# Kernel tuning notes

Measured on AMD Instinct MI355X. Metric: run time of the kernel, lower is better.

Reference implementation:

```python
import jax, jax.numpy as jnp
import numpy as np

N_NODES = 256
N_BAGS = 4
BAG_SIZE = 64


def _conv1d(x, w, b):
    # x: [B, C, T], w: [O, I, K], 'same' padding (pad=1, k=3), stride 1
    y = jax.lax.conv_general_dilated(x, w, window_strides=(1,), padding=[(1, 1)],
                                     dimension_numbers=('NCH', 'OIH', 'NCH'))
    return y + b[None, :, None]


def _select_indices(attention, degree):
    # Deterministic analogue of subgraphSelection: top-4 nodes by degree; for each,
    # prob row hrl = (row + row) * 100 (original numpy graph[:][b] is also row b);
    # pick 64 globally-distinct indices (collision avoidance) by probability, sorted.
    _, b4 = jax.lax.top_k(degree, N_BAGS)
    taken = jnp.zeros(N_NODES, dtype=bool)
    rows = []
    for i in range(N_BAGS):  # fixed small loop
        probs = 200.0 * attention[b4[i]]
        masked = jnp.where(taken, -jnp.inf, probs)
        _, idx = jax.lax.top_k(masked, BAG_SIZE)
        idx = jnp.sort(idx)
        taken = taken.at[idx].set(True)
        rows.append(idx)
    return jnp.stack(rows)  # [4, 64] int32


def setup_inputs() -> dict:
    key = jax.random.key(0)
    ks = jax.random.split(key, 13)
    B, T = 32768, N_NODES
    return {
        'attention': jax.random.uniform(ks[0], (N_NODES, N_NODES), jnp.float32),
        'degree': jax.random.uniform(ks[1], (N_NODES,), jnp.float32),
        'x': jax.random.normal(ks[2], (B, T, 1), jnp.float32),
        'conv1_w': jax.random.normal(ks[3], (1, 1, 3), jnp.float32) * 0.01,
        'conv1_b': jnp.zeros((1,), jnp.float32),
        'W1': jax.random.normal(ks[4], (64, 64), jnp.float32) * 0.05,
        'b1': jnp.zeros((64,), jnp.float32),
        'W2': jax.random.normal(ks[5], (64, 64), jnp.float32) * 0.05,
        'b2': jnp.zeros((64,), jnp.float32),
        'Wa': jax.random.normal(ks[6], (64, 64), jnp.float32) * 0.05,
        'ba': jnp.zeros((64,), jnp.float32),
        'conv2_w': jax.random.normal(ks[7], (4, 4, 3), jnp.float32) * 0.01,
        'conv2_b': jnp.zeros((4,), jnp.float32),
    }


def reference(attention, degree, x, conv1_w, conv1_b, W1, b1, W2, b2, Wa, ba, conv2_w, conv2_b):
    idx = _select_indices(attention, degree)            # [4, 64]
    xp = jnp.transpose(x, (0, 2, 1))                    # [B, 1, T]
    # Conv1D_feature_extracter(1,1,3): tanh(dropout(tanh(conv))) -> eval-mode tanh(tanh(conv))
    x_site = jnp.tanh(jnp.tanh(_conv1d(xp, conv1_w, conv1_b)))  # [B, 1, T]
    # mapping_converge: irregular gather x[b, 0, idx] -> [B, 4, 64]
    mx = xp[:, 0, :][:, idx]
    # IMILmask (torch Linear: y = x W^T + b)
    l1 = jax.nn.relu(mx @ W1.T + b1)
    l2 = jax.nn.relu(mx @ W2.T + b2)
    A_imi = jax.nn.sigmoid((l1 + l2) @ Wa.T + ba)
    masked_x = (A_imi + 1.0) * mx                       # [B, 4, 64]
    # Conv1D_feature_extracter(4,4,3)
    x_bag = jnp.tanh(jnp.tanh(_conv1d(masked_x, conv2_w, conv2_b)))  # [B, 4, 64]
    return (x_bag, x_site)
```

## Files before the change

### kernel.cpp

```cpp
#include <hip/hip_runtime.h>
#include <hip/hip_bf16.h>
#include <math.h>


#define NB 16

typedef __bf16 bf16x8 __attribute__((ext_vector_type(8)));
typedef float  f32x4  __attribute__((ext_vector_type(4)));

__device__ __forceinline__ float tanh_poly(float y) {
    float y2 = y * y;
    float p = fmaf(y2, -0.008863829f, 0.021869488f);
    p = fmaf(y2, p, -0.053968254f);
    p = fmaf(y2, p, 0.13333334f);
    p = fmaf(y2, p, -0.33333334f);
    p = fmaf(y2, p, 1.0f);
    return y * p;
}
__device__ __forceinline__ float dtanh2(float y) { return tanh_poly(tanh_poly(y)); }

__global__ __launch_bounds__(1024) void sel_kernel(
    const float* __restrict__ att, const float* __restrict__ deg,
    int* __restrict__ permg)
{
    __shared__ float pv[256];
    __shared__ int taken[256];
    __shared__ int part[256][5];
    __shared__ int b4s[4];
    __shared__ unsigned long long wmask[4];

    const int tid  = threadIdx.x;
    const int j    = tid & 255;
    const int q    = tid >> 8;
    const int lane = tid & 63;
    const int wv   = tid >> 6;

    if (tid < 256) { taken[tid] = 0; pv[tid] = deg[tid]; }
    __syncthreads();

    for (int rnd = -1; rnd < 4; ++rnd) {
        if (rnd >= 0) {
            if (tid < 256) {
                float p = 200.0f * att[b4s[rnd] * 256 + tid];
                pv[tid] = taken[tid] ? -__builtin_huge_valf() : p;
            }
            __syncthreads();
        }
        {
            float pj = pv[j];
            int cnt = 0;
            const int base = q * 64;
            #pragma unroll 4
            for (int k0 = 0; k0 < 64; ++k0) {
                int k = base + k0;
                float pk = pv[k];
                cnt += (pk > pj || (pk == pj && k < j)) ? 1 : 0;
            }
            part[j][q] = cnt;
        }
        __syncthreads();
        int sel = 0;
        if (tid < 256) {
            int rank = part[tid][0] + part[tid][1] + part[tid][2] + part[tid][3];
            if (rnd < 0) {
                if (rank < 4) b4s[rank] = tid;
            } else {
                sel = (rank < 64) ? 1 : 0;
            }
        }
        if (rnd >= 0) {
            unsigned long long mask = __ballot(sel);
            if (lane == 0 && wv < 4) wmask[wv] = mask;
            __syncthreads();
            if (sel) {
                int pos = __popcll(mask & ((1ull << lane) - 1ull));
                #pragma unroll
                for (int w = 0; w < 4; ++w) if (w < wv) pos += __popcll(wmask[w]);
                permg[rnd * 64 + pos] = tid;
                taken[tid] = 1;
            }
        }
        __syncthreads();
    }
}

__global__ __launch_bounds__(256, 2) void main_kernel(
    const float* __restrict__ x,
    const float* __restrict__ c1w, const float* __restrict__ c1b,
    const float* __restrict__ W1,  const float* __restrict__ b1,
    const float* __restrict__ W2,  const float* __restrict__ b2,
    const float* __restrict__ Wa,  const float* __restrict__ ba,
    const float* __restrict__ c2w, const float* __restrict__ c2b,
    const int* __restrict__ permg,
    float* __restrict__ out, int Btot)
{
    __shared__ float xls[NB][264];
    __shared__ bf16x8 w12f[8][2][64];
    __shared__ bf16x8 w3f[4][2][64];
    __shared__ int perm[256];
    __shared__ __align__(16) unsigned char scratch[4][4352];

    const int tid = threadIdx.x;
    const int batch0 = blockIdx.x * NB;

    #pragma unroll
    for (int i = 0; i < 4; ++i) {
        int flat = i * 1024 + tid * 4;
        int r = flat >> 8, c = flat & 255;
        const float4 v = *(const float4*)&x[(size_t)(batch0 + r) * 256 + c];
        *(float4*)&xls[r][c] = v;
    }
    #pragma unroll
    for (int ii = 0; ii < 4; ++ii) {
        int id = tid + 256 * ii;
        int ct = id >> 7, h = (id >> 6) & 1, l2 = id & 63;
        int n = ct * 16 + (l2 & 15);
        int k = h * 32 + (l2 >> 4) * 8;
        const float* src = (n < 64) ? (W1 + n * 64 + k) : (W2 + (n - 64) * 64 + k);
        float4 u = *(const float4*)src;
        float4 v = *(const float4*)(src + 4);
        bf16x8 f;
        f[0]=(__bf16)u.x; f[1]=(__bf16)u.y; f[2]=(__bf16)u.z; f[3]=(__bf16)u.w;
        f[4]=(__bf16)v.x; f[5]=(__bf16)v.y; f[6]=(__bf16)v.z; f[7]=(__bf16)v.w;
        w12f[ct][h][l2] = f;
    }
    #pragma unroll
    for (int ii = 0; ii < 2; ++ii) {
        int id = tid + 256 * ii;
        int ct = id >> 7, h = (id >> 6) & 1, l2 = id & 63;
        int n = ct * 16 + (l2 & 15);
        int k = h * 32 + (l2 >> 4) * 8;
        const float* src = Wa + n * 64 + k;
        float4 u = *(const float4*)src;
        float4 v = *(const float4*)(src + 4);
        bf16x8 f;
        f[0]=(__bf16)u.x; f[1]=(__bf16)u.y; f[2]=(__bf16)u.z; f[3]=(__bf16)u.w;
        f[4]=(__bf16)v.x; f[5]=(__bf16)v.y; f[6]=(__bf16)v.z; f[7]=(__bf16)v.w;
        w3f[ct][h][l2] = f;
    }
    perm[tid & 255] = permg[tid & 255];
    __syncthreads();

    {
        const float cw0 = c1w[0], cw1 = c1w[1], cw2 = c1w[2], cb = c1b[0];
        const size_t siteBase = (size_t)Btot * 256;
        #pragma unroll
        for (int i = 0; i < 4; ++i) {
            int flat = i * 1024 + tid * 4;
            int r = flat >> 8, c = flat & 255;
            const float* xr = &xls[r][0];
            float xm = (c > 0)       ? xr[c - 1] : 0.0f;
            float x0 = xr[c], x1 = xr[c + 1], x2 = xr[c + 2], x3 = xr[c + 3];
            float xp = (c + 4 < 256) ? xr[c + 4] : 0.0f;
            float4 o4;
            o4.x = dtanh2(fmaf(cw0, xm, fmaf(cw1, x0, fmaf(cw2, x1, cb))));
            o4.y = dtanh2(fmaf(cw0, x0, fmaf(cw1, x1, fmaf(cw2, x2, cb))));
            o4.z = dtanh2(fmaf(cw0, x1, fmaf(cw1, x2, fmaf(cw2, x3, cb))));
            o4.w = dtanh2(fmaf(cw0, x2, fmaf(cw1, x3, fmaf(cw2, xp, cb))));
            *(float4*)&out[siteBase + (size_t)(batch0 + r) * 256 + c] = o4;
        }
    }

    const int l = tid & 63, wvi = tid >> 6;
    const int hi = l >> 4, m = l & 15;

    float b1v[4], b2v[4], bav[4];
    #pragma unroll
    for (int ct = 0; ct < 4; ++ct) {
        b1v[ct] = b1[ct * 16 + m];
        b2v[ct] = b2[ct * 16 + m];
        bav[ct] = ba[ct * 16 + m];
    }

    const int bag = m & 3;
    const int bL  = wvi * 4 + (m >> 2);
    bf16x8 af0, af1;
    #pragma unroll
    for (int jj = 0; jj < 8; ++jj) {
        int k0 = hi * 8 + jj;
        af0[jj] = (__bf16)xls[bL][perm[bag * 64 + k0]];
        af1[jj] = (__bf16)xls[bL][perm[bag * 64 + 32 + k0]];
    }

    f32x4 acc12[8];
    #pragma unroll
    for (int ct = 0; ct < 8; ++ct) acc12[ct] = (f32x4){0.f, 0.f, 0.f, 0.f};
    #pragma unroll
    for (int ct = 0; ct < 8; ++ct) {
        acc12[ct] = __builtin_amdgcn_mfma_f32_16x16x32_bf16(af0, w12f[ct][0][l], acc12[ct], 0, 0, 0);
        acc12[ct] = __builtin_amdgcn_mfma_f32_16x16x32_bf16(af1, w12f[ct][1][l], acc12[ct], 0, 0, 0);
    }

    __bf16* lsb = (__bf16*)scratch[wvi];
    #pragma unroll
    for (int ct = 0; ct < 4; ++ct) {
        #pragma unroll
        for (int qq = 0; qq < 4; ++qq) {
            float a = acc12[ct][qq] + b1v[ct];      a = a > 0.f ? a : 0.f;
            float b = acc12[ct + 4][qq] + b2v[ct];  b = b > 0.f ? b : 0.f;
            lsb[(hi * 4 + qq) * 72 + ct * 16 + m] = (__bf16)(a + b);
        }
    }
    bf16x8 a30 = *(const bf16x8*)(lsb + m * 72 + hi * 8);
    bf16x8 a31 = *(const bf16x8*)(lsb + m * 72 + 32 + hi * 8);

    f32x4 acc3[4];
    #pragma unroll
    for (int ct = 0; ct < 4; ++ct) acc3[ct] = (f32x4){0.f, 0.f, 0.f, 0.f};
    #pragma unroll
    for (int ct = 0; ct < 4; ++ct) {
        acc3[ct] = __builtin_amdgcn_mfma_f32_16x16x32_bf16(a30, w3f[ct][0][l], acc3[ct], 0, 0, 0);
        acc3[ct] = __builtin_amdgcn_mfma_f32_16x16x32_bf16(a31, w3f[ct][1][l], acc3[ct], 0, 0, 0);
    }

    __syncthreads();

    float* msk = (float*)scratch[wvi];
    #pragma unroll
    for (int ct = 0; ct < 4; ++ct) {
        #pragma unroll
        for (int qq = 0; qq < 4; ++qq) {
            float v = acc3[ct][qq] + bav[ct];
            float s = __builtin_amdgcn_rcpf(1.0f + __expf(-v)) + 1.0f;
            int r  = hi * 4 + qq;
            int bq = r >> 2, ii = r & 3;
            int t  = ct * 16 + m;
            float mxv = xls[wvi * 4 + bq][perm[ii * 64 + t]];
            msk[(bq * 4 + ii) * 68 + t] = s * mxv;
        }
    }

    {
        const int bq2 = m >> 2, o = m & 3;
        const int tseg = hi * 16;
        float wv2[4][3];
        #pragma unroll
        for (int ii = 0; ii < 4; ++ii)
            #pragma unroll
            for (int kk = 0; kk < 3; ++kk)
                wv2[ii][kk] = c2w[o * 12 + ii * 3 + kk];
        const float cb2 = c2b[o];

        float mrow[4][16], mm1[4], mp1[4];
        #pragma unroll
        for (int ii = 0; ii < 4; ++ii) {
            const float* base = msk + (bq2 * 4 + ii) * 68;
            #pragma unroll
            for (int ch = 0; ch < 4; ++ch) {
                float4 vv = *(const float4*)(base + tseg + ch * 4);
                mrow[ii][ch * 4 + 0] = vv.x; mrow[ii][ch * 4 + 1] = vv.y;
                mrow[ii][ch * 4 + 2] = vv.z; mrow[ii][ch * 4 + 3] = vv.w;
            }
            mm1[ii] = (tseg > 0)       ? base[tseg - 1]  : 0.0f;
            mp1[ii] = (tseg + 16 < 64) ? base[tseg + 16] : 0.0f;
        }

        float res[16];
        #pragma unroll
        for (int t = 0; t < 16; ++t) {
            float a = cb2;
            #pragma unroll
            for (int ii = 0; ii < 4; ++ii) {
                float xm = (t == 0)  ? mm1[ii] : mrow[ii][t - 1];
                float xc = mrow[ii][t];
                float xp = (t == 15) ? mp1[ii] : mrow[ii][t + 1];
                a = fmaf(wv2[ii][0], xm, a);
                a = fmaf(wv2[ii][1], xc, a);
                a = fmaf(wv2[ii][2], xp, a);
            }
            res[t] = dtanh2(a);
        }
        float* op = out + (size_t)(batch0 + wvi * 4 + bq2) * 256 + o * 64 + tseg;
        #pragma unroll
        for (int ch = 0; ch < 4; ++ch) {
            float4 o4 = { res[ch*4+0], res[ch*4+1], res[ch*4+2], res[ch*4+3] };
            *(float4*)(op + ch * 4) = o4;
        }
    }
}

extern "C" void kernel_launch(void* const* d_in, const int* in_sizes, int n_in,
                              void* d_out, int out_size, void* d_ws, size_t ws_size,
                              hipStream_t stream)
{
    const float* att = (const float*)d_in[0];
    const float* deg = (const float*)d_in[1];
    const float* x   = (const float*)d_in[2];
    const float* c1w = (const float*)d_in[3];
    const float* c1b = (const float*)d_in[4];
    const float* W1  = (const float*)d_in[5];
    const float* b1  = (const float*)d_in[6];
    const float* W2  = (const float*)d_in[7];
    const float* b2  = (const float*)d_in[8];
    const float* Wa  = (const float*)d_in[9];
    const float* ba  = (const float*)d_in[10];
    const float* c2w = (const float*)d_in[11];
    const float* c2b = (const float*)d_in[12];
    float* out = (float*)d_out;
    int* perm  = (int*)d_ws;
    int Btot   = in_sizes[2] / 256;

    hipLaunchKernelGGL(sel_kernel, dim3(1), dim3(1024), 0, stream, att, deg, perm);
    hipLaunchKernelGGL(main_kernel, dim3(Btot / NB), dim3(256), 0, stream,
                       x, c1w, c1b, W1, b1, W2, b2, Wa, ba, c2w, c2b,
                       perm, out, Btot);
}
```

Baseline: 157.6 us.

## Precompute bf16 weight fragments once in prologue kernel, read from global in main

Moves the per-block fp32-to-bf16 conversion of W1/W2/Wa into a second block of the selection kernel, which writes pre-swizzled MFMA fragments to workspace. The main kernel reads the B fragments directly from global/L2 instead of staging them in LDS. This removes redundant conversion work and about 24KB of LDS per block, and the launch bound rises to 4 blocks per CU. The selection kernel's rank loop also now reads LDS as float4. The cost is that MFMA operands now come from global loads through cache, which may add latency. The workspace must also be large enough to hold the fragments.

```diff
diff --git a/kernel.cpp b/kernel.cpp
--- a/kernel.cpp
+++ b/kernel.cpp
@@ -19,17 +19,48 @@
 }
 __device__ __forceinline__ float dtanh2(float y) { return tanh_poly(tanh_poly(y)); }
 
+__device__ __forceinline__ bf16x8 cvt_frag(const float* src) {
+    float4 u = *(const float4*)src;
+    float4 v = *(const float4*)(src + 4);
+    bf16x8 f;
+    f[0]=(__bf16)u.x; f[1]=(__bf16)u.y; f[2]=(__bf16)u.z; f[3]=(__bf16)u.w;
+    f[4]=(__bf16)v.x; f[5]=(__bf16)v.y; f[6]=(__bf16)v.z; f[7]=(__bf16)v.w;
+    return f;
+}
+
 __global__ __launch_bounds__(1024) void sel_kernel(
     const float* __restrict__ att, const float* __restrict__ deg,
+    const float* __restrict__ W1, const float* __restrict__ W2,
+    const float* __restrict__ Wa,
     int* __restrict__ permg)
 {
-    __shared__ float pv[256];
+    const int tid = threadIdx.x;
+
+    if (blockIdx.x == 1) {
+        bf16x8* w12g = (bf16x8*)(permg + 256);
+        bf16x8* w3g  = w12g + 1024;
+        {
+            int ct = tid >> 7, h = (tid >> 6) & 1, l2 = tid & 63;
+            int n = ct * 16 + (l2 & 15);
+            int k = h * 32 + (l2 >> 4) * 8;
+            const float* src = (n < 64) ? (W1 + n * 64 + k) : (W2 + (n - 64) * 64 + k);
+            w12g[ct * 128 + h * 64 + l2] = cvt_frag(src);
+        }
+        if (tid < 512) {
+            int ct = tid >> 7, h = (tid >> 6) & 1, l2 = tid & 63;
+            int n = ct * 16 + (l2 & 15);
+            int k = h * 32 + (l2 >> 4) * 8;
+            w3g[ct * 128 + h * 64 + l2] = cvt_frag(Wa + n * 64 + k);
+        }
+        return;
+    }
+
+    __shared__ __align__(16) float pv[256];
     __shared__ int taken[256];
     __shared__ int part[256][5];
     __shared__ int b4s[4];
     __shared__ unsigned long long wmask[4];
 
-    const int tid  = threadIdx.x;
     const int j    = tid & 255;
     const int q    = tid >> 8;
     const int lane = tid & 63;
@@ -49,12 +80,15 @@
         {
             float pj = pv[j];
             int cnt = 0;
-            const int base = q * 64;
-            #pragma unroll 4
-            for (int k0 = 0; k0 < 64; ++k0) {
-                int k = base + k0;
-                float pk = pv[k];
-                cnt += (pk > pj || (pk == pj && k < j)) ? 1 : 0;
+            const float4* pv4 = (const float4*)&pv[q * 64];
+            #pragma unroll
+            for (int k4 = 0; k4 < 16; ++k4) {
+                float4 v = pv4[k4];
+                int kb = q * 64 + k4 * 4;
+                cnt += (v.x > pj || (v.x == pj && (kb + 0) < j)) ? 1 : 0;
+                cnt += (v.y > pj || (v.y == pj && (kb + 1) < j)) ? 1 : 0;
+                cnt += (v.z > pj || (v.z == pj && (kb + 2) < j)) ? 1 : 0;
+                cnt += (v.w > pj || (v.w == pj && (kb + 3) < j)) ? 1 : 0;
             }
             part[j][q] = cnt;
         }
@@ -84,24 +118,23 @@
     }
 }
 
-__global__ __launch_bounds__(256, 2) void main_kernel(
+__global__ __launch_bounds__(256, 4) void main_kernel(
     const float* __restrict__ x,
     const float* __restrict__ c1w, const float* __restrict__ c1b,
-    const float* __restrict__ W1,  const float* __restrict__ b1,
-    const float* __restrict__ W2,  const float* __restrict__ b2,
-    const float* __restrict__ Wa,  const float* __restrict__ ba,
+    const float* __restrict__ b1,  const float* __restrict__ b2,
+    const float* __restrict__ ba,
     const float* __restrict__ c2w, const float* __restrict__ c2b,
     const int* __restrict__ permg,
     float* __restrict__ out, int Btot)
 {
     __shared__ float xls[NB][264];
-    __shared__ bf16x8 w12f[8][2][64];
-    __shared__ bf16x8 w3f[4][2][64];
     __shared__ int perm[256];
     __shared__ __align__(16) unsigned char scratch[4][4352];
 
     const int tid = threadIdx.x;
     const int batch0 = blockIdx.x * NB;
+    const bf16x8* __restrict__ w12g = (const bf16x8*)(permg + 256);
+    const bf16x8* __restrict__ w3g  = w12g + 1024;
 
     #pragma unroll
     for (int i = 0; i < 4; ++i) {
@@ -110,35 +143,7 @@
         const float4 v = *(const float4*)&x[(size_t)(batch0 + r) * 256 + c];
         *(float4*)&xls[r][c] = v;
     }
-    #pragma unroll
-    for (int ii = 0; ii < 4; ++ii) {
-        int id = tid + 256 * ii;
-        int ct = id >> 7, h = (id >> 6) & 1, l2 = id & 63;
-        int n = ct * 16 + (l2 & 15);
-        int k = h * 32 + (l2 >> 4) * 8;
-        const float* src = (n < 64) ? (W1 + n * 64 + k) : (W2 + (n - 64) * 64 + k);
-        float4 u = *(const float4*)src;
-        float4 v = *(const float4*)(src + 4);
-        bf16x8 f;
-        f[0]=(__bf16)u.x; f[1]=(__bf16)u.y; f[2]=(__bf16)u.z; f[3]=(__bf16)u.w;
-        f[4]=(__bf16)v.x; f[5]=(__bf16)v.y; f[6]=(__bf16)v.z; f[7]=(__bf16)v.w;
-        w12f[ct][h][l2] = f;
-    }
-    #pragma unroll
-    for (int ii = 0; ii < 2; ++ii) {
-        int id = tid + 256 * ii;
-        int ct = id >> 7, h = (id >> 6) & 1, l2 = id & 63;
-        int n = ct * 16 + (l2 & 15);
-        int k = h * 32 + (l2 >> 4) * 8;
-        const float* src = Wa + n * 64 + k;
-        float4 u = *(const float4*)src;
-        float4 v = *(const float4*)(src + 4);
-        bf16x8 f;
-        f[0]=(__bf16)u.x; f[1]=(__bf16)u.y; f[2]=(__bf16)u.z; f[3]=(__bf16)u.w;
-        f[4]=(__bf16)v.x; f[5]=(__bf16)v.y; f[6]=(__bf16)v.z; f[7]=(__bf16)v.w;
-        w3f[ct][h][l2] = f;
-    }
-    perm[tid & 255] = permg[tid & 255];
+    perm[tid] = permg[tid];
     __syncthreads();
 
     {
@@ -187,8 +192,10 @@
     for (int ct = 0; ct < 8; ++ct) acc12[ct] = (f32x4){0.f, 0.f, 0.f, 0.f};
     #pragma unroll
     for (int ct = 0; ct < 8; ++ct) {
-        acc12[ct] = __builtin_amdgcn_mfma_f32_16x16x32_bf16(af0, w12f[ct][0][l], acc12[ct], 0, 0, 0);
-        acc12[ct] = __builtin_amdgcn_mfma_f32_16x16x32_bf16(af1, w12f[ct][1][l], acc12[ct], 0, 0, 0);
+        bf16x8 bf0 = w12g[ct * 128 + l];
+        bf16x8 bf1 = w12g[ct * 128 + 64 + l];
+        acc12[ct] = __builtin_amdgcn_mfma_f32_16x16x32_bf16(af0, bf0, acc12[ct], 0, 0, 0);
+        acc12[ct] = __builtin_amdgcn_mfma_f32_16x16x32_bf16(af1, bf1, acc12[ct], 0, 0, 0);
     }
 
     __bf16* lsb = (__bf16*)scratch[wvi];
@@ -209,8 +216,10 @@
     for (int ct = 0; ct < 4; ++ct) acc3[ct] = (f32x4){0.f, 0.f, 0.f, 0.f};
     #pragma unroll
     for (int ct = 0; ct < 4; ++ct) {
-        acc3[ct] = __builtin_amdgcn_mfma_f32_16x16x32_bf16(a30, w3f[ct][0][l], acc3[ct], 0, 0, 0);
-        acc3[ct] = __builtin_amdgcn_mfma_f32_16x16x32_bf16(a31, w3f[ct][1][l], acc3[ct], 0, 0, 0);
+        bf16x8 bf0 = w3g[ct * 128 + l];
+        bf16x8 bf1 = w3g[ct * 128 + 64 + l];
+        acc3[ct] = __builtin_amdgcn_mfma_f32_16x16x32_bf16(a30, bf0, acc3[ct], 0, 0, 0);
+        acc3[ct] = __builtin_amdgcn_mfma_f32_16x16x32_bf16(a31, bf1, acc3[ct], 0, 0, 0);
     }
 
     __syncthreads();
@@ -300,8 +309,9 @@
     int* perm  = (int*)d_ws;
     int Btot   = in_sizes[2] / 256;
 
-    hipLaunchKernelGGL(sel_kernel, dim3(1), dim3(1024), 0, stream, att, deg, perm);
+    hipLaunchKernelGGL(sel_kernel, dim3(2), dim3(1024), 0, stream,
+                       att, deg, W1, W2, Wa, perm);
     hipLaunchKernelGGL(main_kernel, dim3(Btot / NB), dim3(256), 0, stream,
-                       x, c1w, c1b, W1, b1, W2, b2, Wa, ba, c2w, c2b,
+                       x, c1w, c1b, b1, b2, ba, c2w, c2b,
                        perm, out, Btot);
 }
```

New measurement: 142.5 us. 1.11x faster.
